# Kernel optimization log

Hardware: AMD Instinct MI355X
Metric: run time of the kernel (lower is better)

Reference implementation:

```python
import jax, jax.numpy as jnp
import numpy as np

NUM_HEADS = 16

def setup_inputs() -> dict:
    key = jax.random.key(0)
    k1, k2, k3 = jax.random.split(key, 3)
    B, S, H = 2, 2048, 1024
    x = jax.random.normal(k1, (B, S, H), dtype=jnp.float32)
    w_qkv = jax.random.normal(k2, (H, 3 * H), dtype=jnp.float32) * (1.0 / np.sqrt(H))
    w_out = jax.random.normal(k3, (H, H), dtype=jnp.float32) * (1.0 / np.sqrt(H))
    return {"x": x, "w_qkv": w_qkv, "w_out": w_out}

def reference(x, w_qkv, w_out):
    B, S, H = x.shape
    nh = NUM_HEADS
    dh = H // nh
    qkv = x @ w_qkv  # (B, S, 3H)
    q, k, v = jnp.split(qkv, 3, axis=-1)
    # (B, nh, S, dh)
    q = q.reshape(B, S, nh, dh).transpose(0, 2, 1, 3)
    k = k.reshape(B, S, nh, dh).transpose(0, 2, 1, 3)
    v = v.reshape(B, S, nh, dh).transpose(0, 2, 1, 3)
    att = jnp.einsum('bhsd,bhSd->bhsS', q, k) / np.sqrt(dh).astype(np.float32)
    causal = jnp.tril(jnp.ones((S, S), dtype=bool))
    att = jnp.where(causal[None, None], att, -jnp.inf)
    att = jax.nn.softmax(att, axis=-1)
    out = jnp.einsum('bhsS,bhSd->bhsd', att, v)
    out = out.transpose(0, 2, 1, 3).reshape(B, S, H)
    return out @ w_out
```

## Files before the change

kernel.cpp:

```cpp
#include <hip/hip_runtime.h>

#define DEVINL __device__ __forceinline__

typedef __attribute__((ext_vector_type(8)))  __bf16         bf16x8;
typedef __attribute__((ext_vector_type(4)))  float          f32x4;
typedef __attribute__((ext_vector_type(16))) float          f32x16;
typedef __attribute__((ext_vector_type(8)))  unsigned short ushort8;
typedef __attribute__((ext_vector_type(4)))  unsigned short ushort4v;
typedef __attribute__((ext_vector_type(4)))  unsigned int   uint4v;
typedef __attribute__((ext_vector_type(4)))  float          float4v;

DEVINL unsigned short f2bf(float f) {
  unsigned int u = __float_as_uint(f);
  u += 0x7fffu + ((u >> 16) & 1u);
  return (unsigned short)(u >> 16);
}

DEVINL float bf2f(unsigned short u) {
  return __uint_as_float(((unsigned int)u) << 16);
}

DEVINL bf16x8 ldbf8(const unsigned short* p) {
  return __builtin_bit_cast(bf16x8, *(const ushort8*)p);
}

DEVINL unsigned cvtpk_bf16(float lo, float hi) {
  unsigned r;
  asm("v_cvt_pk_bf16_f32 %0, %1, %2" : "=v"(r) : "v"(lo), "v"(hi));
  return r;
}

DEVINL void gload_lds16(const unsigned short* g, unsigned short* l) {
  __builtin_amdgcn_global_load_lds((const __attribute__((address_space(1))) void*)g,
                                   (__attribute__((address_space(3))) void*)l, 16, 0, 0);
}

__global__ __launch_bounds__(256) void prepass_kernel(
    const float* __restrict__ x, const float* __restrict__ w_qkv,
    const float* __restrict__ w_out, unsigned short* __restrict__ xb,
    unsigned short* __restrict__ wqkvT, unsigned short* __restrict__ woutT) {
  __shared__ float tile[32][33];
  const int B = blockIdx.x;
  if (B < 1024) {
    const int n4 = 1048576;
    for (int i = B * 256 + threadIdx.x; i < n4; i += 1024 * 256) {
      float4v v = *(const float4v*)(x + (size_t)4 * i);
      ushort4v o;
      o[0] = f2bf(v[0]); o[1] = f2bf(v[1]); o[2] = f2bf(v[2]); o[3] = f2bf(v[3]);
      *(ushort4v*)(xb + (size_t)4 * i) = o;
    }
    return;
  }
  const float* in; unsigned short* out; int C, bx, by;
  if (B < 4096) { const int idx = B - 1024; bx = idx % 96; by = idx / 96; in = w_qkv; out = wqkvT; C = 3072; }
  else          { const int idx = B - 4096; bx = idx & 31; by = idx >> 5; in = w_out; out = woutT; C = 1024; }
  const int R = 1024;
  const int tx = threadIdx.x & 31, ty = threadIdx.x >> 5;
  const int r0 = by << 5, c0 = bx << 5;
#pragma unroll
  for (int i = 0; i < 32; i += 8)
    tile[ty + i][tx] = in[(size_t)(r0 + ty + i) * C + (c0 + tx)];
  __syncthreads();
#pragma unroll
  for (int i = 0; i < 32; i += 8)
    out[(size_t)(c0 + ty + i) * R + (r0 + tx)] = f2bf(tile[tx][ty + i]);
}

template <bool OUT_BF16>
__global__ __launch_bounds__(256, 3) void gemm_bt_kernel(
    const unsigned short* __restrict__ A,
    const unsigned short* __restrict__ Bt,
    void* __restrict__ Cout,
    int M, int N, int K, int lda, int ldb, int ldc,
    unsigned short* __restrict__ VtOut) {
  __shared__ __align__(16) unsigned short As[2][128 * 32];
  __shared__ __align__(16) unsigned short Bs[2][128 * 32];
  const int tid = threadIdx.x;
  const int lane = tid & 63, wave = tid >> 6;
  const int wr = wave >> 1, wc = wave & 1;
  const int g = lane >> 4, q = lane & 15;
  const int row0 = blockIdx.x << 7, col0 = blockIdx.y << 7;

  const int srow = tid >> 2;
  const int sg = ((tid & 3) ^ (srow & 3)) << 3;
  const unsigned short* Ap0 = A + (size_t)(row0 + srow) * lda + sg;
  const unsigned short* Ap1 = Ap0 + (size_t)64 * lda;
  const unsigned short* Bp0 = Bt + (size_t)(col0 + srow) * ldb + sg;
  const unsigned short* Bp1 = Bp0 + (size_t)64 * ldb;

  f32x4 acc[4][4] = {};

  gload_lds16(Ap0, &As[0][wave * 512]);
  gload_lds16(Ap1, &As[0][2048 + wave * 512]);
  gload_lds16(Bp0, &Bs[0][wave * 512]);
  gload_lds16(Bp1, &Bs[0][2048 + wave * 512]);

  const int gx = (g ^ (q & 3)) << 3;
  const int nk = K >> 5;
  int cur = 0;

  for (int t = 0; t < nk; ++t) {
    if (t + 1 < nk) {
      Ap0 += 32; Ap1 += 32; Bp0 += 32; Bp1 += 32;
      gload_lds16(Ap0, &As[cur ^ 1][wave * 512]);
      gload_lds16(Ap1, &As[cur ^ 1][2048 + wave * 512]);
      gload_lds16(Bp0, &Bs[cur ^ 1][wave * 512]);
      gload_lds16(Bp1, &Bs[cur ^ 1][2048 + wave * 512]);
      asm volatile("s_waitcnt vmcnt(4)" ::: "memory");
    } else {
      asm volatile("s_waitcnt vmcnt(0)" ::: "memory");
    }
    __builtin_amdgcn_s_barrier();

    bf16x8 af[4], bfr[4];
#pragma unroll
    for (int mb = 0; mb < 4; ++mb)
      af[mb] = ldbf8(&As[cur][(wr * 64 + mb * 16 + q) * 32] + gx);
#pragma unroll
    for (int nb = 0; nb < 4; ++nb)
      bfr[nb] = ldbf8(&Bs[cur][(wc * 64 + nb * 16 + q) * 32] + gx);
#pragma unroll
    for (int mb = 0; mb < 4; ++mb)
#pragma unroll
      for (int nb = 0; nb < 4; ++nb)
        acc[mb][nb] = __builtin_amdgcn_mfma_f32_16x16x32_bf16(af[mb], bfr[nb], acc[mb][nb], 0, 0, 0);

    __builtin_amdgcn_s_barrier();
    cur ^= 1;
  }

  const bool isV = OUT_BF16 && (VtOut != nullptr) && (col0 >= 2048);
#pragma unroll
  for (int mb = 0; mb < 4; ++mb)
#pragma unroll
    for (int nb = 0; nb < 4; ++nb)
#pragma unroll
      for (int r = 0; r < 4; ++r) {
        const int row = row0 + wr * 64 + mb * 16 + g * 4 + r;
        const int col = col0 + wc * 64 + nb * 16 + q;
        const float v = acc[mb][nb][r];
        if (isV) {
          const int cp = col - 2048, hI = cp >> 6, dI = cp & 63;
          VtOut[((size_t)((row >> 11) * 16 + hI) * 64 + dI) * 2048 + (row & 2047)] = f2bf(v);
        } else if (OUT_BF16) {
          ((unsigned short*)Cout)[(size_t)row * ldc + col] = f2bf(v);
        } else {
          ((float*)Cout)[(size_t)row * ldc + col] = v;
        }
      }
}

__global__ __launch_bounds__(256, 3) void gemm_bt64_kernel(
    const unsigned short* __restrict__ A,
    const unsigned short* __restrict__ Bt,
    float* __restrict__ Cout,
    int K, int lda, int ldb, int ldc) {
  __shared__ __align__(16) unsigned short As[2][64 * 32];
  __shared__ __align__(16) unsigned short Bs[2][128 * 32];
  const int tid = threadIdx.x;
  const int lane = tid & 63, wave = tid >> 6;
  const int wr = wave >> 1, wc = wave & 1;
  const int g = lane >> 4, q = lane & 15;
  const int row0 = blockIdx.x << 6, col0 = blockIdx.y << 7;

  const int srow = tid >> 2;
  const int sg = ((tid & 3) ^ (srow & 3)) << 3;
  const unsigned short* Ap = A + (size_t)(row0 + srow) * lda + sg;
  const unsigned short* Bp0 = Bt + (size_t)(col0 + srow) * ldb + sg;
  const unsigned short* Bp1 = Bp0 + (size_t)64 * ldb;

  f32x4 acc[2][4] = {};

  gload_lds16(Ap, &As[0][wave * 512]);
  gload_lds16(Bp0, &Bs[0][wave * 512]);
  gload_lds16(Bp1, &Bs[0][2048 + wave * 512]);

  const int gx = (g ^ (q & 3)) << 3;
  const int nk = K >> 5;
  int cur = 0;

  for (int t = 0; t < nk; ++t) {
    if (t + 1 < nk) {
      Ap += 32; Bp0 += 32; Bp1 += 32;
      gload_lds16(Ap, &As[cur ^ 1][wave * 512]);
      gload_lds16(Bp0, &Bs[cur ^ 1][wave * 512]);
      gload_lds16(Bp1, &Bs[cur ^ 1][2048 + wave * 512]);
      asm volatile("s_waitcnt vmcnt(3)" ::: "memory");
    } else {
      asm volatile("s_waitcnt vmcnt(0)" ::: "memory");
    }
    __builtin_amdgcn_s_barrier();

    bf16x8 af[2], bfr[4];
#pragma unroll
    for (int mb = 0; mb < 2; ++mb)
      af[mb] = ldbf8(&As[cur][(wr * 32 + mb * 16 + q) * 32] + gx);
#pragma unroll
    for (int nb = 0; nb < 4; ++nb)
      bfr[nb] = ldbf8(&Bs[cur][(wc * 64 + nb * 16 + q) * 32] + gx);
#pragma unroll
    for (int mb = 0; mb < 2; ++mb)
#pragma unroll
      for (int nb = 0; nb < 4; ++nb)
        acc[mb][nb] = __builtin_amdgcn_mfma_f32_16x16x32_bf16(af[mb], bfr[nb], acc[mb][nb], 0, 0, 0);

    __builtin_amdgcn_s_barrier();
    cur ^= 1;
  }

#pragma unroll
  for (int mb = 0; mb < 2; ++mb)
#pragma unroll
    for (int nb = 0; nb < 4; ++nb)
#pragma unroll
      for (int r = 0; r < 4; ++r) {
        const int row = row0 + wr * 32 + mb * 16 + g * 4 + r;
        const int col = col0 + wc * 64 + nb * 16 + q;
        Cout[(size_t)row * ldc + col] = acc[mb][nb][r];
      }
}

__global__ __launch_bounds__(256, 2) void attn_kernel(
    const unsigned short* __restrict__ qkv,
    const unsigned short* __restrict__ VtG,
    unsigned short* __restrict__ OlP,
    unsigned short* __restrict__ OhP,
    float* __restrict__ stats) {
  const int S = 2048, H = 1024, LD = 2048;
  const int tid = threadIdx.x;
  const int wave = tid >> 6, lane = tid & 63;
  const int c = lane & 31, hh = lane >> 5;

  const int L = blockIdx.x;
  const int group = L >> 8, r0_ = L & 255;
  const int pairid = r0_ & 7, bh = r0_ >> 3;
  const int qc = (group & 2) ? (15 - pairid) : pairid;
  const int half = group & 1;
  const int b = bh >> 4, h = bh & 15;
  const int q0w = qc * 128 + wave * 32;

  const unsigned short* Qb = qkv + (size_t)b * S * LD + h * 64;
  const unsigned short* Kb = Qb + 1024;
  const unsigned short* Vt = VtG + (size_t)(b * 16 + h) * 64 * S;

  __shared__ __align__(16) unsigned short Ks[2][64 * 64];
  __shared__ __align__(16) unsigned short Vs[2][64 * 64];

  const int srow = lane >> 3;
  const int srcg = ((lane & 7) ^ srow) << 3;
  const int wrow = wave * 8 + srow;

  const int nit = qc + 1;
  const int tb = half ? nit : 0;

  {
    const int cc = tb << 6;
    gload_lds16(Kb + (size_t)(cc + wrow) * LD + srcg,      Ks[0] + wave * 512);
    gload_lds16(Kb + (size_t)(cc + 32 + wrow) * LD + srcg, Ks[0] + 2048 + wave * 512);
    gload_lds16(Vt + (size_t)wrow * S + cc + srcg,         Vs[0] + wave * 512);
    gload_lds16(Vt + (size_t)(32 + wrow) * S + cc + srcg,  Vs[0] + 2048 + wave * 512);
  }

  bf16x8 qf[4];
#pragma unroll
  for (int kc = 0; kc < 4; ++kc)
    qf[kc] = ldbf8(Qb + (size_t)(q0w + c) * LD + kc * 16 + hh * 8);

  f32x16 acc[2] = {};
  float m_r = -1e30f, l_r = 0.f;
  const float CE = 0.125f * 1.44269504f;

  int cur = 0;
  const int swz = (c & 7) << 3;

  for (int t = 0; t < nit; ++t) {
    if (t + 1 < nit) {
      const int c1 = (tb + t + 1) << 6;
      unsigned short* KsN = Ks[cur ^ 1];
      unsigned short* VsN = Vs[cur ^ 1];
      gload_lds16(Kb + (size_t)(c1 + wrow) * LD + srcg,      KsN + wave * 512);
      gload_lds16(Kb + (size_t)(c1 + 32 + wrow) * LD + srcg, KsN + 2048 + wave * 512);
      gload_lds16(Vt + (size_t)wrow * S + c1 + srcg,         VsN + wave * 512);
      gload_lds16(Vt + (size_t)(32 + wrow) * S + c1 + srcg,  VsN + 2048 + wave * 512);
      asm volatile("s_waitcnt vmcnt(4)" ::: "memory");
    } else {
      asm volatile("s_waitcnt vmcnt(0)" ::: "memory");
    }
    __builtin_amdgcn_s_barrier();

    const int c0 = (tb + t) << 6;
    const unsigned short* KsC = Ks[cur];
    const unsigned short* VsC = Vs[cur];

    if (c0 <= q0w + 31) {
      int nv = ((q0w + 31 - c0) >> 5) + 1; if (nv > 2) nv = 2;

      bf16x8 kf[2][4];
#pragma unroll
      for (int n = 0; n < 2; ++n) if (n < nv)
#pragma unroll
        for (int kc = 0; kc < 4; ++kc)
          kf[n][kc] = ldbf8(KsC + (n * 32 + c) * 64 + ((kc * 16 + hh * 8) ^ swz));

      f32x16 st[2] = {};
      __builtin_amdgcn_s_setprio(1);
#pragma unroll
      for (int n = 0; n < 2; ++n) if (n < nv)
#pragma unroll
        for (int kc = 0; kc < 4; ++kc)
          st[n] = __builtin_amdgcn_mfma_f32_32x32x16_bf16(kf[n][kc], qf[kc], st[n], 0, 0, 0);
      __builtin_amdgcn_s_setprio(0);

      bf16x8 vf[2][4];
#pragma unroll
      for (int db = 0; db < 2; ++db)
#pragma unroll
        for (int kk = 0; kk < 4; ++kk) if (kk < 2 * nv)
          vf[db][kk] = ldbf8(VsC + (db * 32 + c) * 64 + ((kk * 16 + hh * 8) ^ swz));

      if (c0 + 63 > q0w) {
#pragma unroll
        for (int n = 0; n < 2; ++n) if (n < nv)
#pragma unroll
          for (int r = 0; r < 16; ++r) {
            const int kv = c0 + n * 32 + (r & 3) + 8 * (r >> 2) + 4 * hh;
            if (kv > q0w + c) st[n][r] = -1e30f;
          }
      }

      f32x4 pm = {-1e30f, -1e30f, -1e30f, -1e30f};
#pragma unroll
      for (int n = 0; n < 2; ++n) if (n < nv)
#pragma unroll
        for (int r = 0; r < 16; ++r) pm[r & 3] = fmaxf(pm[r & 3], st[n][r]);
      const float pmax = fmaxf(fmaxf(pm[0], pm[1]), fmaxf(pm[2], pm[3]));
      if (!__all(pmax <= m_r + 64.f)) {
        float px = fmaxf(pmax, __shfl_xor(pmax, 32));
        const float mn = fmaxf(m_r, px);
        const float sf = __builtin_amdgcn_exp2f((m_r - mn) * CE);
        m_r = mn; l_r *= sf;
#pragma unroll
        for (int db = 0; db < 2; ++db) acc[db] *= sf;
      }
      const float mC = m_r * CE;
      f32x4 la = {0.f, 0.f, 0.f, 0.f};
#pragma unroll
      for (int n = 0; n < 2; ++n) if (n < nv)
#pragma unroll
        for (int r = 0; r < 16; ++r) {
          const float p = __builtin_amdgcn_exp2f(fmaf(st[n][r], CE, -mC));
          st[n][r] = p;
          la[r & 3] += p;
        }
      l_r += (la[0] + la[1]) + (la[2] + la[3]);

      bf16x8 pa[4];
#pragma unroll
      for (int n = 0; n < 2; ++n) if (n < nv) {
        unsigned T0 = cvtpk_bf16(st[n][0],  st[n][1]);
        unsigned T1 = cvtpk_bf16(st[n][2],  st[n][3]);
        unsigned T2 = cvtpk_bf16(st[n][4],  st[n][5]);
        unsigned T3 = cvtpk_bf16(st[n][6],  st[n][7]);
        unsigned T4 = cvtpk_bf16(st[n][8],  st[n][9]);
        unsigned T5 = cvtpk_bf16(st[n][10], st[n][11]);
        unsigned T6 = cvtpk_bf16(st[n][12], st[n][13]);
        unsigned T7 = cvtpk_bf16(st[n][14], st[n][15]);
        asm("v_permlane32_swap_b32 %0, %1" : "+v"(T0), "+v"(T2));
        asm("v_permlane32_swap_b32 %0, %1" : "+v"(T1), "+v"(T3));
        asm("v_permlane32_swap_b32 %0, %1" : "+v"(T4), "+v"(T6));
        asm("v_permlane32_swap_b32 %0, %1" : "+v"(T5), "+v"(T7));
        uint4v w0; w0[0] = T0; w0[1] = T1; w0[2] = T2; w0[3] = T3;
        uint4v w1; w1[0] = T4; w1[1] = T5; w1[2] = T6; w1[3] = T7;
        pa[2 * n]     = __builtin_bit_cast(bf16x8, w0);
        pa[2 * n + 1] = __builtin_bit_cast(bf16x8, w1);
      }

      __builtin_amdgcn_s_setprio(1);
#pragma unroll
      for (int kk = 0; kk < 4; ++kk) if (kk < 2 * nv)
#pragma unroll
        for (int db = 0; db < 2; ++db)
          acc[db] = __builtin_amdgcn_mfma_f32_32x32x16_bf16(vf[db][kk], pa[kk], acc[db], 0, 0, 0);
      __builtin_amdgcn_s_setprio(0);
    }

    __builtin_amdgcn_s_barrier();
    cur ^= 1;
  }

  const float lt = l_r + __shfl_xor(l_r, 32);
  const float inv = lt > 0.f ? 1.f / lt : 0.f;
  unsigned short* Op = half ? OhP : OlP;
  const size_t rowbase = (size_t)(b * S + q0w + c) * H + h * 64;
#pragma unroll
  for (int db = 0; db < 2; ++db)
#pragma unroll
    for (int blk = 0; blk < 4; ++blk) {
      ushort4v o;
#pragma unroll
      for (int j = 0; j < 4; ++j) o[j] = f2bf(acc[db][blk * 4 + j] * inv);
      *(ushort4v*)(Op + rowbase + db * 32 + blk * 8 + hh * 4) = o;
    }
  if (hh == 0) {
    float* sp = stats + ((((size_t)(b * 16 + h)) << 11) + q0w + c) * 4 + (half ? 2 : 0);
    sp[0] = m_r; sp[1] = lt;
  }
}

__global__ __launch_bounds__(256) void attn_merge_kernel(
    const unsigned short* __restrict__ Ol,
    const unsigned short* __restrict__ Oh,
    const float* __restrict__ stats,
    unsigned short* __restrict__ Oout) {
  const float CE = 0.125f * 1.44269504f;
  const int i = blockIdx.x * 256 + threadIdx.x;
  const int r = i >> 7;
  const int g8 = i & 127;
  const int h = g8 >> 3;
  const int s = r & 2047, b = r >> 11;
  const float4v st = *(const float4v*)(stats + ((((size_t)(b * 16 + h)) << 11) + s) * 4);
  const float mn = fmaxf(st[0], st[2]);
  const float wl_ = st[1] * __builtin_amdgcn_exp2f((st[0] - mn) * CE);
  const float wh_ = st[3] * __builtin_amdgcn_exp2f((st[2] - mn) * CE);
  const float inv = 1.f / (wl_ + wh_);
  const float wl = wl_ * inv, wh = wh_ * inv;
  const size_t off = (size_t)i * 8;
  const ushort8 a = *(const ushort8*)(Ol + off);
  const ushort8 cc = *(const ushort8*)(Oh + off);
  ushort8 o;
#pragma unroll
  for (int j = 0; j < 8; ++j)
    o[j] = f2bf(wl * bf2f(a[j]) + wh * bf2f(cc[j]));
  *(ushort8*)(Oout + off) = o;
}

extern "C" void kernel_launch(void* const* d_in, const int* in_sizes, int n_in,
                              void* d_out, int out_size, void* d_ws, size_t ws_size,
                              hipStream_t stream) {
  const float* x     = (const float*)d_in[0];
  const float* w_qkv = (const float*)d_in[1];
  const float* w_out = (const float*)d_in[2];
  const int B = 2, S = 2048, H = 1024;
  const int M = B * S;

  unsigned short* xb    = (unsigned short*)d_ws;
  unsigned short* wqkvT = xb + (size_t)M * H;
  unsigned short* woutT = wqkvT + (size_t)3 * H * H;
  unsigned short* qkb   = woutT + (size_t)H * H;
  unsigned short* VtG   = qkb + (size_t)M * 2048;
  unsigned short* Ob    = VtG + (size_t)B * 16 * 64 * S;
  unsigned short* OhP   = xb;
  float*          stats = (float*)wqkvT;

  prepass_kernel<<<5120, 256, 0, stream>>>(x, w_qkv, w_out, xb, wqkvT, woutT);

  gemm_bt_kernel<true><<<dim3(M / 128, (3 * H) / 128), 256, 0, stream>>>(
      xb, wqkvT, qkb, M, 3 * H, H, H, H, 2048, VtG);

  attn_kernel<<<1024, 256, 0, stream>>>(qkb, VtG, Ob, OhP, stats);

  attn_merge_kernel<<<2048, 256, 0, stream>>>(Ob, OhP, stats, Ob);

  gemm_bt64_kernel<<<dim3(M / 64, H / 128), 256, 0, stream>>>(
      Ob, woutT, (float*)d_out, H, H, H, H);
}
```

Baseline: 116.6 us.

## Stage V-transpose epilogue through LDS and strengthen LDS swizzle

The V-output epilogue of the QKV GEMM is rewritten to first write the accumulator tile transposed into shared memory, then emit coalesced 16-byte row stores into the Vt buffer instead of scattered 2-byte strided writes. Separately, the LDS XOR swizzle in both GEMM kernels now also mixes bits 2-3 of the row index, to reduce bank conflicts on the fragment reads. The transpose adds two block barriers and reuses the staging buffers. A transposed 2-byte write pattern into LDS may itself hit bank conflicts.

```diff
diff --git a/kernel.cpp b/kernel.cpp
--- a/kernel.cpp
+++ b/kernel.cpp
@@ -73,8 +73,9 @@
     void* __restrict__ Cout,
     int M, int N, int K, int lda, int ldb, int ldc,
     unsigned short* __restrict__ VtOut) {
-  __shared__ __align__(16) unsigned short As[2][128 * 32];
-  __shared__ __align__(16) unsigned short Bs[2][128 * 32];
+  __shared__ __align__(16) unsigned short smem[2][2][128 * 32];
+  unsigned short (*As)[128 * 32] = smem[0];
+  unsigned short (*Bs)[128 * 32] = smem[1];
   const int tid = threadIdx.x;
   const int lane = tid & 63, wave = tid >> 6;
   const int wr = wave >> 1, wc = wave & 1;
@@ -82,7 +83,7 @@
   const int row0 = blockIdx.x << 7, col0 = blockIdx.y << 7;
 
   const int srow = tid >> 2;
-  const int sg = ((tid & 3) ^ (srow & 3)) << 3;
+  const int sg = ((tid & 3) ^ (srow & 3) ^ ((srow >> 2) & 3)) << 3;
   const unsigned short* Ap0 = A + (size_t)(row0 + srow) * lda + sg;
   const unsigned short* Ap1 = Ap0 + (size_t)64 * lda;
   const unsigned short* Bp0 = Bt + (size_t)(col0 + srow) * ldb + sg;
@@ -95,7 +96,7 @@
   gload_lds16(Bp0, &Bs[0][wave * 512]);
   gload_lds16(Bp1, &Bs[0][2048 + wave * 512]);
 
-  const int gx = (g ^ (q & 3)) << 3;
+  const int gx = (g ^ (q & 3) ^ (q >> 2)) << 3;
   const int nk = K >> 5;
   int cur = 0;
 
@@ -130,6 +131,30 @@
   }
 
   const bool isV = OUT_BF16 && (VtOut != nullptr) && (col0 >= 2048);
+  if (isV) {
+    unsigned short* T = &smem[0][0][0];
+    __syncthreads();
+#pragma unroll
+    for (int mb = 0; mb < 4; ++mb)
+#pragma unroll
+      for (int nb = 0; nb < 4; ++nb)
+#pragma unroll
+        for (int r = 0; r < 4; ++r) {
+          const int sr = wr * 64 + mb * 16 + g * 4 + r;
+          const int dc = wc * 64 + nb * 16 + q;
+          T[dc * 128 + sr] = f2bf(acc[mb][nb][r]);
+        }
+    __syncthreads();
+    const int d = tid >> 1, sh = (tid & 1) << 6;
+    const int hI = ((col0 - 2048) >> 6) + (d >> 6), dI = d & 63;
+    unsigned short* dst = VtOut + ((size_t)((row0 >> 11) * 16 + hI) * 64 + dI) * 2048 +
+                          (row0 & 2047) + sh;
+    const unsigned short* src = T + d * 128 + sh;
+#pragma unroll
+    for (int j = 0; j < 8; ++j)
+      *(ushort8*)(dst + j * 8) = *(const ushort8*)(src + j * 8);
+    return;
+  }
 #pragma unroll
   for (int mb = 0; mb < 4; ++mb)
 #pragma unroll
@@ -139,14 +164,8 @@
         const int row = row0 + wr * 64 + mb * 16 + g * 4 + r;
         const int col = col0 + wc * 64 + nb * 16 + q;
         const float v = acc[mb][nb][r];
-        if (isV) {
-          const int cp = col - 2048, hI = cp >> 6, dI = cp & 63;
-          VtOut[((size_t)((row >> 11) * 16 + hI) * 64 + dI) * 2048 + (row & 2047)] = f2bf(v);
-        } else if (OUT_BF16) {
-          ((unsigned short*)Cout)[(size_t)row * ldc + col] = f2bf(v);
-        } else {
-          ((float*)Cout)[(size_t)row * ldc + col] = v;
-        }
+        if (OUT_BF16) ((unsigned short*)Cout)[(size_t)row * ldc + col] = f2bf(v);
+        else          ((float*)Cout)[(size_t)row * ldc + col] = v;
       }
 }
 
@@ -164,7 +183,7 @@
   const int row0 = blockIdx.x << 6, col0 = blockIdx.y << 7;
 
   const int srow = tid >> 2;
-  const int sg = ((tid & 3) ^ (srow & 3)) << 3;
+  const int sg = ((tid & 3) ^ (srow & 3) ^ ((srow >> 2) & 3)) << 3;
   const unsigned short* Ap = A + (size_t)(row0 + srow) * lda + sg;
   const unsigned short* Bp0 = Bt + (size_t)(col0 + srow) * ldb + sg;
   const unsigned short* Bp1 = Bp0 + (size_t)64 * ldb;
@@ -175,7 +194,7 @@
   gload_lds16(Bp0, &Bs[0][wave * 512]);
   gload_lds16(Bp1, &Bs[0][2048 + wave * 512]);
 
-  const int gx = (g ^ (q & 3)) << 3;
+  const int gx = (g ^ (q & 3) ^ (q >> 2)) << 3;
   const int nk = K >> 5;
   int cur = 0;
 
```

Measured after the change: 114.5 us, median of 2. About the same (-1.7%).
